# Optimization experiments

Measured on AMD Instinct MI355X. Metric: run time of the kernel, lower is better.

Reference implementation:

```python
import jax, jax.numpy as jnp
import numpy as np

N_NODES = 50000
N_EDGES = 800000
D_IN = 96
D_OUT = 96


def setup_inputs() -> dict:
    key = jax.random.key(0)
    k1, k2, k3, k4 = jax.random.split(key, 4)
    feat = jax.random.normal(k1, (N_NODES, D_IN), dtype=jnp.float32)
    # xavier_normal-like init for weight, zeros bias (as in the torch module)
    std = (2.0 / (D_IN + D_OUT)) ** 0.5
    weight = jax.random.normal(k2, (D_IN, D_OUT), dtype=jnp.float32) * std
    bias = jnp.zeros((D_OUT,), dtype=jnp.float32)
    src = jax.random.randint(k3, (N_EDGES,), 0, N_NODES, dtype=jnp.int64)
    dst = jax.random.randint(k4, (N_EDGES,), 0, N_NODES, dtype=jnp.int64)
    return {"feat": feat, "weight": weight, "bias": bias, "src": src, "dst": dst}


def reference(feat, weight, bias, src, dst):
    N = feat.shape[0]
    ones = jnp.ones(src.shape[0], dtype=feat.dtype)
    out_deg = jax.ops.segment_sum(ones, src, num_segments=N)  # out-degree per node
    in_deg = jax.ops.segment_sum(ones, dst, num_segments=N)   # in-degree per node
    ci = jnp.clip(out_deg, 1.0, None) ** -0.5                 # src-side norm
    cj = jnp.clip(in_deg, 1.0, None) ** -0.5                  # dst-side norm
    # gather src features * ci, scatter-sum to dst, scale by cj
    msg = feat[src] * ci[src, None]                           # [E, D_IN]
    agg = jax.ops.segment_sum(msg, dst, num_segments=N) * cj[:, None]
    # DGL UDF reduce only updates nodes that receive messages; isolated
    # (zero in-degree) nodes keep their original features.
    h = jnp.where(in_deg[:, None] > 0, agg, feat)
    return jnp.matmul(h, weight) + bias
```

## Files before the change

kernel.cpp:

```cpp
#include <hip/hip_runtime.h>

#define N_NODES 50000
#define N_EDGES 800000
#define D 96
#define D4 (D / 4)

#define RL 12
#define HPAD 13
#define CONV_BLOCKS ((N_NODES * RL + 255) / 256)
#define WPREP_BLOCKS ((D * (D / 2) + 255) / 256)

#define NB 196
#define ECAP 5120
#define SCAP 5120
#define CCAP 6144
#define PA_BLOCKS 256
#define PA_CHUNK 3125

typedef __attribute__((ext_vector_type(8))) short short8;
typedef __attribute__((ext_vector_type(4))) float floatx4;

__device__ __forceinline__ short8 as_short8(uint4 u) { return *(short8*)&u; }

__device__ __forceinline__ unsigned bf16pack(float a, float b) {
    unsigned ua = __float_as_uint(a);
    unsigned ub = __float_as_uint(b);
    ua = (ua + 0x7FFFu + ((ua >> 16) & 1u)) >> 16;
    ub = (ub + 0x7FFFu + ((ub >> 16) & 1u)) & 0xFFFF0000u;
    return ua | ub;
}

__global__ void __launch_bounds__(1024) sortA_kernel(
        const int* __restrict__ src, const int* __restrict__ dst,
        unsigned* __restrict__ gcur,
        unsigned* __restrict__ ebuf, unsigned short* __restrict__ sbuf) {
    __shared__ unsigned raw[PA_CHUNK];
    __shared__ unsigned ord[PA_CHUNK];
    __shared__ unsigned short sord[PA_CHUNK];
    __shared__ unsigned hist[512];
    __shared__ unsigned sc[512], lstart[512], cur[512], gbase[512];
    int t = threadIdx.x;
    int e0 = blockIdx.x * PA_CHUNK;
    if (t < 512) hist[t] = 0;
    __syncthreads();
    for (int i = t; i < PA_CHUNK; i += 1024) {
        int s = src[e0 + i];
        int d = dst[e0 + i];
        raw[i] = ((unsigned)d << 16) | (unsigned)s;
        atomicAdd(&hist[d >> 8], 1u);
        atomicAdd(&hist[256 + (s >> 8)], 1u);
    }
    __syncthreads();
    if (t < 512) sc[t] = hist[t];
    __syncthreads();
    for (int o = 1; o < 256; o <<= 1) {
        unsigned v = 0;
        if (t < 512 && (t & 255) >= o) v = sc[t - o];
        __syncthreads();
        if (t < 512 && (t & 255) >= o) sc[t] += v;
        __syncthreads();
    }
    if (t < 512) {
        unsigned ls = sc[t] - hist[t];
        lstart[t] = ls;
        cur[t] = ls;
        if ((t & 255) < NB)
            gbase[t] = atomicAdd(&gcur[(t >> 8) * NB + (t & 255)], hist[t]);
    }
    __syncthreads();
    for (int i = t; i < PA_CHUNK; i += 1024) {
        unsigned r = raw[i];
        unsigned p = atomicAdd(&cur[r >> 24], 1u);
        ord[p] = r;
        unsigned s = r & 0xFFFFu;
        unsigned q = atomicAdd(&cur[256 + (s >> 8)], 1u);
        sord[q] = (unsigned short)s;
    }
    __syncthreads();
    for (int i = t; i < PA_CHUNK; i += 1024) {
        unsigned r = ord[i];
        unsigned bd = r >> 24;
        unsigned pos = gbase[bd] + ((unsigned)i - lstart[bd]);
        if (pos < ECAP) ebuf[bd * ECAP + pos] = r;
        unsigned s = sord[i];
        unsigned bs = 256 + (s >> 8);
        unsigned pos2 = gbase[bs] + ((unsigned)i - lstart[bs]);
        if (pos2 < SCAP) sbuf[(size_t)(bs - 256) * SCAP + pos2] = (unsigned short)s;
    }
}

__global__ void __launch_bounds__(1024) sortB_kernel(
        const unsigned* __restrict__ gcur, const unsigned* __restrict__ ebuf,
        const unsigned short* __restrict__ sbuf,
        int* __restrict__ deg_out, int* __restrict__ deg_in,
        int* __restrict__ off, unsigned short* __restrict__ csr) {
    __shared__ unsigned eb[ECAP];
    __shared__ unsigned short csr_l[CCAP];
    __shared__ unsigned dcount[256], dcur[256], scount[256], sc[256];
    int b = blockIdx.x;
    int t = threadIdx.x;
    unsigned cntd = gcur[b];      if (cntd > ECAP) cntd = ECAP;
    unsigned cnts = gcur[NB + b]; if (cnts > SCAP) cnts = SCAP;
    if (t < 256) { dcount[t] = 0; scount[t] = 0; }
    __syncthreads();
    const unsigned* __restrict__ sg = ebuf + (size_t)b * ECAP;
    for (int i = t; i < (int)cntd; i += 1024) {
        unsigned r = sg[i];
        eb[i] = r;
        atomicAdd(&dcount[(r >> 16) & 255u], 1u);
    }
    const unsigned short* __restrict__ ss = sbuf + (size_t)b * SCAP;
    for (int i = t; i < (int)cnts; i += 1024)
        atomicAdd(&scount[ss[i] & 255u], 1u);
    __syncthreads();
    if (t < 256) sc[t] = (dcount[t] + 7u) & ~7u;
    __syncthreads();
    for (int o = 1; o < 256; o <<= 1) {
        unsigned v = 0;
        if (t < 256 && t >= o) v = sc[t - o];
        __syncthreads();
        if (t < 256 && t >= o) sc[t] += v;
        __syncthreads();
    }
    if (t < 256) {
        int n = b * 256 + t;
        unsigned ex = sc[t] - ((dcount[t] + 7u) & ~7u);
        dcur[t] = ex;
        if (n < N_NODES) {
            deg_in[n]  = (int)dcount[t];
            deg_out[n] = (int)scount[t];
            off[n] = b * CCAP + (int)ex;
        }
    }
    __syncthreads();
    for (int i = t; i < (int)cntd; i += 1024) {
        unsigned r = eb[i];
        unsigned p = atomicAdd(&dcur[(r >> 16) & 255u], 1u);
        if (p < CCAP) csr_l[p] = (unsigned short)(r & 0xFFFFu);
    }
    __syncthreads();
    unsigned tot = sc[255];
    if (tot > CCAP) tot = CCAP;
    unsigned* __restrict__ og = (unsigned*)(csr + (size_t)b * CCAP);
    const unsigned* __restrict__ cl = (const unsigned*)csr_l;
    for (int i = t; i < (int)(tot >> 1); i += 1024) og[i] = cl[i];
}

__global__ void __launch_bounds__(256) conv_kernel(
        const float4* __restrict__ feat4, const int* __restrict__ deg_out,
        uint4* __restrict__ sfeat, const float* __restrict__ W,
        unsigned* __restrict__ WT32) {
    int blk = blockIdx.x;
    if (blk >= CONV_BLOCKS) {
        int t = (blk - CONV_BLOCKS) * 256 + threadIdx.x;
        if (t >= D * (D / 2)) return;
        int n = t / (D / 2);
        int j = t - n * (D / 2);
        float w0 = W[(2 * j) * D + n];
        float w1 = W[(2 * j + 1) * D + n];
        WT32[n * (D / 2) + j] = bf16pack(w0, w1);
        return;
    }
    int t = blk * 256 + threadIdx.x;
    if (t >= N_NODES * RL) return;
    int n = t / RL;
    int lane = t - n * RL;
    float c = rsqrtf(fmaxf((float)deg_out[n], 1.0f));
    float4 a = feat4[n * D4 + lane * 2];
    float4 b = feat4[n * D4 + lane * 2 + 1];
    uint4 o;
    o.x = bf16pack(a.x * c, a.y * c);
    o.y = bf16pack(a.z * c, a.w * c);
    o.z = bf16pack(b.x * c, b.y * c);
    o.w = bf16pack(b.z * c, b.w * c);
    sfeat[t] = o;
}

__global__ void __launch_bounds__(192) gather_mm_kernel(
        const float4* __restrict__ feat4, const uint4* __restrict__ sfeat,
        const int* __restrict__ deg_in, const int* __restrict__ off,
        const unsigned short* __restrict__ csr, const uint4* __restrict__ wt4,
        const float* __restrict__ bias, float* __restrict__ out) {
    __shared__ uint4 sh[16 * HPAD];
    int tid = threadIdx.x;
    {
        int g = tid / RL;
        int lane = tid - g * RL;
        int n = blockIdx.x * 16 + g;
        int deg = deg_in[n];
        uint4* __restrict__ hout = &sh[g * HPAD + lane];
        if (deg == 0) {
            float4 a = feat4[n * D4 + lane * 2];
            float4 b = feat4[n * D4 + lane * 2 + 1];
            uint4 o;
            o.x = bf16pack(a.x, a.y);
            o.y = bf16pack(a.z, a.w);
            o.z = bf16pack(b.x, b.y);
            o.w = bf16pack(b.z, b.w);
            *hout = o;
        } else {
            const unsigned short* __restrict__ bk = csr + off[n];
            const uint4* __restrict__ sf = sfeat + lane;
            float acc[8] = {};
#define ACC8(v)  { \
        acc[0] += __uint_as_float((v).x << 16); \
        acc[1] += __uint_as_float((v).x & 0xFFFF0000u); \
        acc[2] += __uint_as_float((v).y << 16); \
        acc[3] += __uint_as_float((v).y & 0xFFFF0000u); \
        acc[4] += __uint_as_float((v).z << 16); \
        acc[5] += __uint_as_float((v).z & 0xFFFF0000u); \
        acc[6] += __uint_as_float((v).w << 16); \
        acc[7] += __uint_as_float((v).w & 0xFFFF0000u); }
            int i = 0;
            int full16 = deg & ~15;
            for (; i < full16; i += 16) {
                uint4 ia = *(const uint4*)(bk + i);
                uint4 ib = *(const uint4*)(bk + i + 8);
                unsigned s0 = ia.x & 0xFFFFu, s1 = ia.x >> 16;
                unsigned s2 = ia.y & 0xFFFFu, s3 = ia.y >> 16;
                unsigned s4 = ia.z & 0xFFFFu, s5 = ia.z >> 16;
                unsigned s6 = ia.w & 0xFFFFu, s7 = ia.w >> 16;
                unsigned s8 = ib.x & 0xFFFFu, s9 = ib.x >> 16;
                unsigned sa = ib.y & 0xFFFFu, sb = ib.y >> 16;
                unsigned sx = ib.z & 0xFFFFu, sd = ib.z >> 16;
                unsigned se = ib.w & 0xFFFFu, sfi = ib.w >> 16;
                uint4 v0 = sf[(size_t)s0 * RL];
                uint4 v1 = sf[(size_t)s1 * RL];
                uint4 v2 = sf[(size_t)s2 * RL];
                uint4 v3 = sf[(size_t)s3 * RL];
                uint4 v4 = sf[(size_t)s4 * RL];
                uint4 v5 = sf[(size_t)s5 * RL];
                uint4 v6 = sf[(size_t)s6 * RL];
                uint4 v7 = sf[(size_t)s7 * RL];
                uint4 v8 = sf[(size_t)s8 * RL];
                uint4 v9 = sf[(size_t)s9 * RL];
                uint4 va = sf[(size_t)sa * RL];
                uint4 vb = sf[(size_t)sb * RL];
                uint4 vc = sf[(size_t)sx * RL];
                uint4 vd = sf[(size_t)sd * RL];
                uint4 ve = sf[(size_t)se * RL];
                uint4 vf = sf[(size_t)sfi * RL];
                ACC8(v0); ACC8(v1); ACC8(v2); ACC8(v3);
                ACC8(v4); ACC8(v5); ACC8(v6); ACC8(v7);
                ACC8(v8); ACC8(v9); ACC8(va); ACC8(vb);
                ACC8(vc); ACC8(vd); ACC8(ve); ACC8(vf);
            }
            int full8 = deg & ~7;
            for (; i < full8; i += 8) {
                uint4 idx = *(const uint4*)(bk + i);
                unsigned s0 = idx.x & 0xFFFFu, s1 = idx.x >> 16;
                unsigned s2 = idx.y & 0xFFFFu, s3 = idx.y >> 16;
                unsigned s4 = idx.z & 0xFFFFu, s5 = idx.z >> 16;
                unsigned s6 = idx.w & 0xFFFFu, s7 = idx.w >> 16;
                uint4 v0 = sf[(size_t)s0 * RL];
                uint4 v1 = sf[(size_t)s1 * RL];
                uint4 v2 = sf[(size_t)s2 * RL];
                uint4 v3 = sf[(size_t)s3 * RL];
                uint4 v4 = sf[(size_t)s4 * RL];
                uint4 v5 = sf[(size_t)s5 * RL];
                uint4 v6 = sf[(size_t)s6 * RL];
                uint4 v7 = sf[(size_t)s7 * RL];
                ACC8(v0); ACC8(v1); ACC8(v2); ACC8(v3);
                ACC8(v4); ACC8(v5); ACC8(v6); ACC8(v7);
            }
            for (; i < deg; ++i) {
                uint4 v = sf[(size_t)bk[i] * RL];
                ACC8(v);
            }
#undef ACC8
            float cj = rsqrtf((float)deg);
            uint4 o;
            o.x = bf16pack(acc[0] * cj, acc[1] * cj);
            o.y = bf16pack(acc[2] * cj, acc[3] * cj);
            o.z = bf16pack(acc[4] * cj, acc[5] * cj);
            o.w = bf16pack(acc[6] * cj, acc[7] * cj);
            *hout = o;
        }
    }
    __syncthreads();
    int wave = tid >> 6;
    int lane = tid & 63;
    int m = lane & 15, quad = lane >> 4;
    short8 a0 = as_short8(sh[m * HPAD + quad]);
    short8 a1 = as_short8(sh[m * HPAD + 4 + quad]);
    short8 a2 = as_short8(sh[m * HPAD + 8 + quad]);
    int row0 = blockIdx.x * 16;
    int r_out0 = row0 + quad * 4;
#pragma unroll
    for (int ct = wave * 2; ct < wave * 2 + 2; ++ct) {
        int n = ct * 16 + m;
        int wb = n * RL + quad;
        short8 b0 = as_short8(wt4[wb]);
        short8 b1 = as_short8(wt4[wb + 4]);
        short8 b2 = as_short8(wt4[wb + 8]);
        floatx4 c = {0.f, 0.f, 0.f, 0.f};
        c = __builtin_amdgcn_mfma_f32_16x16x32_bf16(a0, b0, c, 0, 0, 0);
        c = __builtin_amdgcn_mfma_f32_16x16x32_bf16(a1, b1, c, 0, 0, 0);
        c = __builtin_amdgcn_mfma_f32_16x16x32_bf16(a2, b2, c, 0, 0, 0);
        float bs = bias[n];
#pragma unroll
        for (int r = 0; r < 4; ++r)
            out[(size_t)(r_out0 + r) * D + n] = c[r] + bs;
    }
}

extern "C" void kernel_launch(void* const* d_in, const int* in_sizes, int n_in,
                              void* d_out, int out_size, void* d_ws, size_t ws_size,
                              hipStream_t stream) {
    const float* feat = (const float*)d_in[0];
    const float* W    = (const float*)d_in[1];
    const float* bias = (const float*)d_in[2];
    const int*   src  = (const int*)d_in[3];
    const int*   dst  = (const int*)d_in[4];

    unsigned*       gcur    = (unsigned*)d_ws;
    int*            deg_out = (int*)(gcur + 2 * NB);
    int*            deg_in  = deg_out + N_NODES;
    int*            off     = deg_in + N_NODES;
    unsigned*       ebuf    = (unsigned*)(off + N_NODES);
    unsigned short* sbuf    = (unsigned short*)(ebuf + (size_t)NB * ECAP);
    unsigned short* csr     = sbuf + (size_t)NB * SCAP;
    uint4*          sfeat   = (uint4*)(csr + (size_t)NB * CCAP);
    unsigned*       WT32    = (unsigned*)(sfeat + (size_t)N_NODES * RL);

    hipMemsetAsync(gcur, 0, 2 * NB * sizeof(unsigned), stream);
    sortA_kernel<<<PA_BLOCKS, 1024, 0, stream>>>(src, dst, gcur, ebuf, sbuf);
    sortB_kernel<<<NB, 1024, 0, stream>>>(gcur, ebuf, sbuf, deg_out, deg_in, off, csr);
    conv_kernel<<<CONV_BLOCKS + WPREP_BLOCKS, 256, 0, stream>>>(
        (const float4*)feat, deg_out, sfeat, W, WT32);
    gather_mm_kernel<<<N_NODES / 16, 192, 0, stream>>>(
        (const float4*)feat, sfeat, deg_in, off, csr, (const uint4*)WT32,
        bias, (float*)d_out);
}
```

Before: 138.8 us.

## Fuse feature conversion into split-bucket CSR build and retune sortA chunking

Merges the per-bucket CSR construction with the bf16 source-feature scaling so the out-degree counts never round-trip through global memory. Each 256-node bucket is now handled by two blocks, each owning 128 nodes, and a shuffle-based scan replaces the shared-memory scan. The weight-transpose prep is folded into the same launch, which removes one kernel launch. sortA also switches to 400 blocks of 2000 edges. In exchange, each half-block reads its whole bucket's edge list and discards half of it, and the edge list is no longer staged in shared memory.

```diff
diff --git a/kernel.cpp b/kernel.cpp
--- a/kernel.cpp
+++ b/kernel.cpp
@@ -7,15 +7,15 @@
 
 #define RL 12
 #define HPAD 13
-#define CONV_BLOCKS ((N_NODES * RL + 255) / 256)
-#define WPREP_BLOCKS ((D * (D / 2) + 255) / 256)
 
 #define NB 196
 #define ECAP 5120
 #define SCAP 5120
-#define CCAP 6144
-#define PA_BLOCKS 256
-#define PA_CHUNK 3125
+#define HCCAP 3072
+#define PA_BLOCKS 400
+#define PA_CHUNK 2000
+#define SB_BLOCKS 392
+#define WPREP_TB 5
 
 typedef __attribute__((ext_vector_type(8))) short short8;
 typedef __attribute__((ext_vector_type(4))) float floatx4;
@@ -92,67 +92,13 @@
 __global__ void __launch_bounds__(1024) sortB_kernel(
         const unsigned* __restrict__ gcur, const unsigned* __restrict__ ebuf,
         const unsigned short* __restrict__ sbuf,
-        int* __restrict__ deg_out, int* __restrict__ deg_in,
-        int* __restrict__ off, unsigned short* __restrict__ csr) {
-    __shared__ unsigned eb[ECAP];
-    __shared__ unsigned short csr_l[CCAP];
-    __shared__ unsigned dcount[256], dcur[256], scount[256], sc[256];
-    int b = blockIdx.x;
-    int t = threadIdx.x;
-    unsigned cntd = gcur[b];      if (cntd > ECAP) cntd = ECAP;
-    unsigned cnts = gcur[NB + b]; if (cnts > SCAP) cnts = SCAP;
-    if (t < 256) { dcount[t] = 0; scount[t] = 0; }
-    __syncthreads();
-    const unsigned* __restrict__ sg = ebuf + (size_t)b * ECAP;
-    for (int i = t; i < (int)cntd; i += 1024) {
-        unsigned r = sg[i];
-        eb[i] = r;
-        atomicAdd(&dcount[(r >> 16) & 255u], 1u);
-    }
-    const unsigned short* __restrict__ ss = sbuf + (size_t)b * SCAP;
-    for (int i = t; i < (int)cnts; i += 1024)
-        atomicAdd(&scount[ss[i] & 255u], 1u);
-    __syncthreads();
-    if (t < 256) sc[t] = (dcount[t] + 7u) & ~7u;
-    __syncthreads();
-    for (int o = 1; o < 256; o <<= 1) {
-        unsigned v = 0;
-        if (t < 256 && t >= o) v = sc[t - o];
-        __syncthreads();
-        if (t < 256 && t >= o) sc[t] += v;
-        __syncthreads();
-    }
-    if (t < 256) {
-        int n = b * 256 + t;
-        unsigned ex = sc[t] - ((dcount[t] + 7u) & ~7u);
-        dcur[t] = ex;
-        if (n < N_NODES) {
-            deg_in[n]  = (int)dcount[t];
-            deg_out[n] = (int)scount[t];
-            off[n] = b * CCAP + (int)ex;
-        }
-    }
-    __syncthreads();
-    for (int i = t; i < (int)cntd; i += 1024) {
-        unsigned r = eb[i];
-        unsigned p = atomicAdd(&dcur[(r >> 16) & 255u], 1u);
-        if (p < CCAP) csr_l[p] = (unsigned short)(r & 0xFFFFu);
-    }
-    __syncthreads();
-    unsigned tot = sc[255];
-    if (tot > CCAP) tot = CCAP;
-    unsigned* __restrict__ og = (unsigned*)(csr + (size_t)b * CCAP);
-    const unsigned* __restrict__ cl = (const unsigned*)csr_l;
-    for (int i = t; i < (int)(tot >> 1); i += 1024) og[i] = cl[i];
-}
-
-__global__ void __launch_bounds__(256) conv_kernel(
-        const float4* __restrict__ feat4, const int* __restrict__ deg_out,
-        uint4* __restrict__ sfeat, const float* __restrict__ W,
-        unsigned* __restrict__ WT32) {
+        const float4* __restrict__ feat4, const float* __restrict__ W,
+        unsigned* __restrict__ WT32,
+        int* __restrict__ deg_in, int* __restrict__ off,
+        unsigned short* __restrict__ csr, uint4* __restrict__ sfeat) {
     int blk = blockIdx.x;
-    if (blk >= CONV_BLOCKS) {
-        int t = (blk - CONV_BLOCKS) * 256 + threadIdx.x;
+    if (blk >= SB_BLOCKS) {
+        int t = (blk - SB_BLOCKS) * 1024 + threadIdx.x;
         if (t >= D * (D / 2)) return;
         int n = t / (D / 2);
         int j = t - n * (D / 2);
@@ -161,19 +107,83 @@
         WT32[n * (D / 2) + j] = bf16pack(w0, w1);
         return;
     }
-    int t = blk * 256 + threadIdx.x;
-    if (t >= N_NODES * RL) return;
-    int n = t / RL;
-    int lane = t - n * RL;
-    float c = rsqrtf(fmaxf((float)deg_out[n], 1.0f));
-    float4 a = feat4[n * D4 + lane * 2];
-    float4 b = feat4[n * D4 + lane * 2 + 1];
-    uint4 o;
-    o.x = bf16pack(a.x * c, a.y * c);
-    o.y = bf16pack(a.z * c, a.w * c);
-    o.z = bf16pack(b.x * c, b.y * c);
-    o.w = bf16pack(b.z * c, b.w * c);
-    sfeat[t] = o;
+    __shared__ unsigned short csr_l[HCCAP];
+    __shared__ unsigned dcount[128], dcur[128], scount[128];
+    __shared__ unsigned wtot, tot_s;
+    int b = blk >> 1;
+    unsigned half = (unsigned)(blk & 1);
+    int t = threadIdx.x;
+    unsigned cntd = gcur[b];      if (cntd > ECAP) cntd = ECAP;
+    unsigned cnts = gcur[NB + b]; if (cnts > SCAP) cnts = SCAP;
+    if (t < 128) { dcount[t] = 0; scount[t] = 0; }
+    __syncthreads();
+    const unsigned* __restrict__ sg = ebuf + (size_t)b * ECAP;
+    for (int i = t; i < (int)cntd; i += 1024) {
+        unsigned loc = (sg[i] >> 16) & 255u;
+        if ((loc >> 7) == half) atomicAdd(&dcount[loc & 127u], 1u);
+    }
+    const unsigned short* __restrict__ ss = sbuf + (size_t)b * SCAP;
+    for (int i = t; i < (int)cnts; i += 1024) {
+        unsigned loc = ss[i] & 255u;
+        if ((loc >> 7) == half) atomicAdd(&scount[loc & 127u], 1u);
+    }
+    __syncthreads();
+    unsigned pad = 0, incl = 0;
+    if (t < 128) {
+        pad = (dcount[t] + 7u) & ~7u;
+        incl = pad;
+        int lane = t & 63;
+#pragma unroll
+        for (int st = 1; st < 64; st <<= 1) {
+            unsigned u = __shfl_up(incl, st, 64);
+            if (lane >= st) incl += u;
+        }
+        if (t == 63) wtot = incl;
+    }
+    __syncthreads();
+    if (t < 128) {
+        if (t >= 64) incl += wtot;
+        unsigned ex = incl - pad;
+        dcur[t] = ex;
+        if (t == 127) tot_s = incl;
+        int n = b * 256 + (int)(half << 7) + t;
+        if (n < N_NODES) {
+            deg_in[n] = (int)dcount[t];
+            off[n] = blk * HCCAP + (int)ex;
+        }
+    }
+    __syncthreads();
+    for (int i = t; i < (int)cntd; i += 1024) {
+        unsigned r = sg[i];
+        unsigned loc = (r >> 16) & 255u;
+        if ((loc >> 7) == half) {
+            unsigned p = atomicAdd(&dcur[loc & 127u], 1u);
+            if (p < HCCAP) csr_l[p] = (unsigned short)(r & 0xFFFFu);
+        }
+    }
+    __syncthreads();
+    unsigned tot = tot_s;
+    if (tot > HCCAP) tot = HCCAP;
+    unsigned* __restrict__ og = (unsigned*)(csr + (size_t)blk * HCCAP);
+    const unsigned* __restrict__ cl = (const unsigned*)csr_l;
+    for (int i = t; i < (int)(tot >> 1); i += 1024) og[i] = cl[i];
+    int base_n = b * 256 + (int)(half << 7);
+    for (int r = t; r < 128 * RL; r += 1024) {
+        int nl = r / RL;
+        int lane = r - nl * RL;
+        int n = base_n + nl;
+        if (n < N_NODES) {
+            float c = rsqrtf(fmaxf((float)scount[nl], 1.0f));
+            float4 a = feat4[(size_t)n * D4 + lane * 2];
+            float4 bb = feat4[(size_t)n * D4 + lane * 2 + 1];
+            uint4 o;
+            o.x = bf16pack(a.x * c, a.y * c);
+            o.y = bf16pack(a.z * c, a.w * c);
+            o.z = bf16pack(bb.x * c, bb.y * c);
+            o.w = bf16pack(bb.z * c, bb.w * c);
+            sfeat[(size_t)n * RL + lane] = o;
+        }
+    }
 }
 
 __global__ void __launch_bounds__(192) gather_mm_kernel(
@@ -314,20 +324,18 @@
     const int*   dst  = (const int*)d_in[4];
 
     unsigned*       gcur    = (unsigned*)d_ws;
-    int*            deg_out = (int*)(gcur + 2 * NB);
-    int*            deg_in  = deg_out + N_NODES;
+    int*            deg_in  = (int*)(gcur + 2 * NB);
     int*            off     = deg_in + N_NODES;
     unsigned*       ebuf    = (unsigned*)(off + N_NODES);
     unsigned short* sbuf    = (unsigned short*)(ebuf + (size_t)NB * ECAP);
     unsigned short* csr     = sbuf + (size_t)NB * SCAP;
-    uint4*          sfeat   = (uint4*)(csr + (size_t)NB * CCAP);
+    uint4*          sfeat   = (uint4*)(csr + (size_t)SB_BLOCKS * HCCAP);
     unsigned*       WT32    = (unsigned*)(sfeat + (size_t)N_NODES * RL);
 
     hipMemsetAsync(gcur, 0, 2 * NB * sizeof(unsigned), stream);
     sortA_kernel<<<PA_BLOCKS, 1024, 0, stream>>>(src, dst, gcur, ebuf, sbuf);
-    sortB_kernel<<<NB, 1024, 0, stream>>>(gcur, ebuf, sbuf, deg_out, deg_in, off, csr);
-    conv_kernel<<<CONV_BLOCKS + WPREP_BLOCKS, 256, 0, stream>>>(
-        (const float4*)feat, deg_out, sfeat, W, WT32);
+    sortB_kernel<<<SB_BLOCKS + WPREP_TB, 1024, 0, stream>>>(
+        gcur, ebuf, sbuf, (const float4*)feat, W, WT32, deg_in, off, csr, sfeat);
     gather_mm_kernel<<<N_NODES / 16, 192, 0, stream>>>(
         (const float4*)feat, sfeat, deg_in, off, csr, (const uint4*)WT32,
         bias, (float*)d_out);
```

New measurement: 139.8 us. Within noise of the previous version (+0.7%).
